# Performance work log

Hardware: AMD Instinct MI355X
Metric: run time of the kernel (lower is better)

Reference implementation:

```python
import jax, jax.numpy as jnp
import numpy as np

N = 100000   # nodes (single node type 'A')
C = 256      # hidden_channels
OUT = 128    # out_channels
E_RAND = 300000  # random edges; total E = N + E_RAND = 400000
LN_EPS = 1e-5


def _linear_params(key, in_c, out_c):
    kw, kb = jax.random.split(key)
    bound = 1.0 / np.sqrt(in_c)
    W = jax.random.uniform(kw, (out_c, in_c), minval=-bound, maxval=bound, dtype=jnp.float32)
    b = jax.random.uniform(kb, (out_c,), minval=-bound, maxval=bound, dtype=jnp.float32)
    return W, b


def _edges(key):
    # guarantee every node appears in both rows -> unique()/remap in the torch
    # code is the identity, so the subgraph equals the full graph
    k0, k1 = jax.random.split(key)
    base = jnp.arange(N, dtype=jnp.int64)
    row0 = jnp.concatenate([base, jax.random.randint(k0, (E_RAND,), 0, N, dtype=jnp.int64)])
    row1 = jnp.concatenate([base, jax.random.randint(k1, (E_RAND,), 0, N, dtype=jnp.int64)])
    return jnp.stack([row0, row1])


def setup_inputs() -> dict:
    key = jax.random.key(0)
    ks = jax.random.split(key, 12)
    x = jax.random.normal(ks[0], (N, C), dtype=jnp.float32)
    edge_index_r0 = _edges(ks[1])
    edge_index_r1 = _edges(ks[2])
    wl0, bl0 = _linear_params(ks[3], C, C)
    w00, b00 = _linear_params(ks[4], C, C)
    w10, b10 = _linear_params(ks[5], C, C)
    wl1, bl1 = _linear_params(ks[6], C, C)
    w01, b01 = _linear_params(ks[7], C, C)
    w11, b11 = _linear_params(ks[8], C, C)
    Wout, bout = _linear_params(ks[9], C, OUT)
    return dict(
        x=x, edge_index_r0=edge_index_r0, edge_index_r1=edge_index_r1,
        wl0=wl0, bl0=bl0, w00=w00, b00=b00, w10=w10, b10=b10,
        gate0=jnp.float32(0.5), lns0=jnp.ones((C,), jnp.float32), lnb0=jnp.zeros((C,), jnp.float32),
        wl1=wl1, bl1=bl1, w01=w01, b01=b01, w11=w11, b11=b11,
        gate1=jnp.float32(0.5), lns1=jnp.ones((C,), jnp.float32), lnb1=jnp.zeros((C,), jnp.float32),
        Wout=Wout, bout=bout,
    )


def _metapath_layer(x0, h, ei, wl, bl, w0, b0, w1, b1, gate, lns, lnb):
    n = h.shape[0]
    src, dst = ei[0], ei[1]
    # PyG flow='target_to_source', aggr='add': message x_j = h[edge_index[1]],
    # scatter-added at edge_index[0]
    agg = jax.ops.segment_sum(h[dst], src, num_segments=n)
    # original code normalizes by bincount of edge_index[1] (kept faithfully)
    deg = jax.ops.segment_sum(jnp.ones_like(dst, dtype=h.dtype), dst, num_segments=n)
    agg = agg / jnp.clip(deg, 1.0)[:, None]
    g = jax.nn.sigmoid(gate)
    out = (agg @ wl.T + bl) + (1.0 - g) * (h @ w0.T + b0) + g * (x0 @ w1.T + b1)
    out = jax.nn.relu(out)
    mu = out.mean(-1, keepdims=True)
    var = out.var(-1, keepdims=True)
    out = (out - mu) / jnp.sqrt(var + LN_EPS) * lns + lnb
    return out  # dropout is identity in eval mode


def reference(x, edge_index_r0, edge_index_r1,
              wl0, bl0, w00, b00, w10, b10, gate0, lns0, lnb0,
              wl1, bl1, w01, b01, w11, b11, gate1, lns1, lnb1,
              Wout, bout):
    x0 = jax.lax.stop_gradient(x)  # x0_dict is detached in the torch code
    h = x
    # metapath is processed in reverse: conv index 1 first, then conv index 0
    h = _metapath_layer(x0, h, edge_index_r1, wl1, bl1, w01, b01, w11, b11, gate1, lns1, lnb1)
    h = _metapath_layer(x0, h, edge_index_r0, wl0, bl0, w00, b00, w10, b10, gate0, lns0, lnb0)
    return h @ Wout.T + bout
```

## Files before the change

kernel.cpp:

```cpp
#include <hip/hip_runtime.h>

typedef unsigned short u16;
typedef unsigned int   u32;

typedef __attribute__((ext_vector_type(8))) __bf16 bf16x8;
typedef __attribute__((ext_vector_type(8))) unsigned short u16x8;
typedef __attribute__((ext_vector_type(4))) float  f32x4;

#define C      256
#define OUTC   128
#define LN_EPS 1e-5f

__device__ __forceinline__ float bf2f(u16 u) {
    u32 i = ((u32)u) << 16; float f; __builtin_memcpy(&f, &i, 4); return f;
}
__device__ __forceinline__ u16 f2bf(float f) {
    u32 i; __builtin_memcpy(&i, &f, 4);
    u32 r = (i + 0x7FFFu + ((i >> 16) & 1u)) >> 16;
    return (u16)r;
}
__device__ __forceinline__ void load_lds16(const void* g, void* l) {
    __builtin_amdgcn_global_load_lds((const __attribute__((address_space(1))) u32*)g,
                                     (__attribute__((address_space(3))) u32*)l, 16, 0, 0);
}
__device__ __forceinline__ int swz(int row) { return (row + (row >> 2)) & 3; }

__global__ void xcast_kernel(const float* __restrict__ x, u16* __restrict__ xb, size_t n8)
{
    size_t i = ((size_t)blockIdx.x * 256 + threadIdx.x);
    if (i >= n8) return;
    const float* p = x + i * 8;
    float4 v0 = *(const float4*)p;
    float4 v1 = *(const float4*)(p + 4);
    u16x8 o;
    o[0] = f2bf(v0.x); o[1] = f2bf(v0.y); o[2] = f2bf(v0.z); o[3] = f2bf(v0.w);
    o[4] = f2bf(v1.x); o[5] = f2bf(v1.y); o[6] = f2bf(v1.z); o[7] = f2bf(v1.w);
    *(u16x8*)(xb + i * 8) = o;
}

__global__ void prep_weights(const float* wl0, const float* w00, const float* w10,
                             const float* bl0, const float* b00, const float* b10,
                             const float* gate0,
                             const float* wl1, const float* w01, const float* w11,
                             const float* bl1, const float* b01, const float* b11,
                             const float* gate1,
                             const float* Wout,
                             u16* __restrict__ WcatA, u16* __restrict__ WcatB,
                             u16* __restrict__ Woutb, float* __restrict__ bcat)
{
    int idx = blockIdx.x * 256 + threadIdx.x;
    float gA = 1.f / (1.f + expf(-gate1[0]));
    float gB = 1.f / (1.f + expf(-gate0[0]));
    if (idx < 256 * 512) {
        int n = idx >> 9, k = idx & 511;
        float v;
        if (k < 256) v = wl1[n * 256 + k];
        else         v = (1.f - gA) * w01[n * 256 + (k - 256)] + gA * w11[n * 256 + (k - 256)];
        WcatA[idx] = f2bf(v);
    } else if (idx < 256 * 512 + 256 * 768) {
        int j = idx - 256 * 512;
        int n = j / 768, k = j - n * 768;
        float v;
        if (k < 256)      v = wl0[n * 256 + k];
        else if (k < 512) v = (1.f - gB) * w00[n * 256 + (k - 256)];
        else              v = gB * w10[n * 256 + (k - 512)];
        WcatB[j] = f2bf(v);
    } else {
        int j = idx - (256 * 512 + 256 * 768);
        if (j < OUTC * C) Woutb[j] = f2bf(Wout[j]);
    }
    if (idx < 512) {
        int nn = idx & 255;
        if (idx < 256) bcat[idx] = bl1[nn] + (1.f - gA) * b01[nn] + gA * b11[nn];
        else           bcat[idx] = bl0[nn] + (1.f - gB) * b00[nn] + gB * b10[nn];
    }
}

__global__ void count_edges(const int* __restrict__ ei, int* __restrict__ counts,
                            int* __restrict__ degcnt, int E, int Nn)
{
    int idx = blockIdx.x * 256 + threadIdx.x;
    if (idx >= E) return;
    int s = ei[idx], d = ei[E + idx];
    if ((unsigned)s >= (unsigned)Nn || (unsigned)d >= (unsigned)Nn) return;
    atomicAdd(counts + s, 1);
    atomicAdd(degcnt + d, 1);
}

__global__ void block_sums(const int* __restrict__ counts, int* __restrict__ partials, int n)
{
    int i = blockIdx.x * 256 + threadIdx.x;
    int v = (i < n) ? counts[i] : 0;
    #pragma unroll
    for (int off = 32; off; off >>= 1) v += __shfl_down(v, off, 64);
    __shared__ int ws[4];
    if ((threadIdx.x & 63) == 0) ws[threadIdx.x >> 6] = v;
    __syncthreads();
    if (threadIdx.x == 0) partials[blockIdx.x] = ws[0] + ws[1] + ws[2] + ws[3];
}

__global__ void scan_partials(int* __restrict__ partials, int nblk)
{
    __shared__ int buf[1024];
    int tid = threadIdx.x;
    int v = (tid < nblk) ? partials[tid] : 0;
    buf[tid] = v; __syncthreads();
    for (int off = 1; off < 1024; off <<= 1) {
        int t = (tid >= off) ? buf[tid - off] : 0;
        __syncthreads();
        buf[tid] += t;
        __syncthreads();
    }
    if (tid < nblk) partials[tid] = buf[tid] - v;
}

__global__ void make_offsets(int* __restrict__ counts_cursor, const int* __restrict__ partials,
                             int* __restrict__ offsets, int n)
{
    __shared__ int buf[256];
    int i = blockIdx.x * 256 + threadIdx.x;
    int cnt = (i < n) ? counts_cursor[i] : 0;
    buf[threadIdx.x] = cnt; __syncthreads();
    for (int off = 1; off < 256; off <<= 1) {
        int t = (threadIdx.x >= off) ? buf[threadIdx.x - off] : 0;
        __syncthreads();
        buf[threadIdx.x] += t;
        __syncthreads();
    }
    int off = partials[blockIdx.x] + buf[threadIdx.x] - cnt;
    if (i < n) {
        offsets[i] = off;
        counts_cursor[i] = off;
        if (i == n - 1) offsets[n] = off + cnt;
    }
}

__global__ void fill_edges(const int* __restrict__ ei, int* __restrict__ cursor,
                           int* __restrict__ edgedst, int E, int Nn)
{
    int idx = blockIdx.x * 256 + threadIdx.x;
    if (idx >= E) return;
    int s = ei[idx], d = ei[E + idx];
    if ((unsigned)s >= (unsigned)Nn || (unsigned)d >= (unsigned)Nn) return;
    int p = atomicAdd(cursor + s, 1);
    edgedst[p] = d;
}

__global__ __launch_bounds__(256) void gather_kernel(
    const int* __restrict__ offsets, const int* __restrict__ edgedst,
    const int* __restrict__ degcnt, const u16* __restrict__ h,
    u16* __restrict__ aggb, int Nn)
{
    int node = blockIdx.x * 4 + (threadIdx.x >> 6);
    if (node >= Nn) return;
    int lane = threadIdx.x & 63;
    int beg = offsets[node], end = offsets[node + 1];
    float4 acc = {0.f, 0.f, 0.f, 0.f};
    for (int e = beg; e < end; ++e) {
        int dst = edgedst[e];
        ushort4 v = *(const ushort4*)(h + (size_t)dst * C + lane * 4);
        acc.x += bf2f(v.x); acc.y += bf2f(v.y);
        acc.z += bf2f(v.z); acc.w += bf2f(v.w);
    }
    float inv = 1.0f / fmaxf((float)degcnt[node], 1.0f);
    ushort4 o;
    o.x = f2bf(acc.x * inv); o.y = f2bf(acc.y * inv);
    o.z = f2bf(acc.z * inv); o.w = f2bf(acc.w * inv);
    *(ushort4*)(aggb + (size_t)node * C + lane * 4) = o;
}

template <int NSEG>
__global__ __launch_bounds__(512, 4) void layer_gemm(
    const u16* __restrict__ s0, const u16* __restrict__ s1, const u16* __restrict__ s2,
    const u16* __restrict__ W,
    const float* __restrict__ bcat,
    const float* __restrict__ lns, const float* __restrict__ lnb,
    u16* __restrict__ Hout, int Nnodes)
{
    constexpr int WK = NSEG * 256;
    constexpr int KT = NSEG * 8;

    __shared__ u16 Alds[128 * 32];
    __shared__ u16 Blds[256 * 32];
    __shared__ float lnpart[128][4][2];

    const int tid  = threadIdx.x;
    const int wave = tid >> 6, lane = tid & 63;
    const int wave_m = wave & 1, wave_n = wave >> 1;
    const int q = lane >> 4, l15 = lane & 15;
    const int m0 = blockIdx.x * 128;

    const int srow = (wave << 4) + (lane >> 2);
    int anode = m0 + srow; if (anode >= Nnodes) anode = Nnodes - 1;
    const int asc = (lane & 3) ^ swz(srow);
    const size_t a_goff = (size_t)anode * C + asc * 8;
    u16* a_ldst = Alds + (wave << 9);

    const u16* bgp[2]; u16* bldst[2];
    #pragma unroll
    for (int i = 0; i < 2; ++i) {
        int cb = wave + i * 8;
        int brow = (cb << 4) + (lane >> 2);
        int bsc = (lane & 3) ^ swz(brow);
        bgp[i]   = W + brow * WK + bsc * 8;
        bldst[i] = Blds + (cb << 9);
    }

    int aoff[4], boff[4];
    #pragma unroll
    for (int t = 0; t < 4; ++t) {
        int ar = wave_m * 64 + t * 16 + l15;
        aoff[t] = ar * 32 + ((q ^ swz(ar)) << 3);
        int br = wave_n * 64 + t * 16 + l15;
        boff[t] = br * 32 + ((q ^ swz(br)) << 3);
    }

    f32x4 acc[4][4] = {};

    for (int kt = 0; kt < KT; ++kt) {
        const u16* Asrc = (kt < 8) ? s0 : ((NSEG == 2 || kt < 16) ? s1 : s2);
        load_lds16(Asrc + a_goff + ((kt & 7) << 5), a_ldst);
        int k0 = kt << 5;
        load_lds16(bgp[0] + k0, bldst[0]);
        load_lds16(bgp[1] + k0, bldst[1]);
        __syncthreads();

        bf16x8 af[4], bfr[4];
        #pragma unroll
        for (int t = 0; t < 4; ++t) af[t]  = *(const bf16x8*)&Alds[aoff[t]];
        #pragma unroll
        for (int f = 0; f < 4; ++f) bfr[f] = *(const bf16x8*)&Blds[boff[f]];
        #pragma unroll
        for (int t = 0; t < 4; ++t)
            #pragma unroll
            for (int f = 0; f < 4; ++f)
                acc[t][f] = __builtin_amdgcn_mfma_f32_16x16x32_bf16(af[t], bfr[f], acc[t][f], 0, 0, 0);
        __syncthreads();
    }

    float bias[4], lsc[4], lbi[4];
    #pragma unroll
    for (int f = 0; f < 4; ++f) {
        int n = wave_n * 64 + f * 16 + l15;
        bias[f] = bcat[n]; lsc[f] = lns[n]; lbi[f] = lnb[n];
    }
    #pragma unroll
    for (int t = 0; t < 4; ++t)
        #pragma unroll
        for (int r = 0; r < 4; ++r) {
            float p = 0.f, pp = 0.f;
            #pragma unroll
            for (int f = 0; f < 4; ++f) {
                float v = acc[t][f][r] + bias[f];
                v = fmaxf(v, 0.f);
                acc[t][f][r] = v;
                p += v; pp += v * v;
            }
            #pragma unroll
            for (int off = 1; off < 16; off <<= 1) {
                p  += __shfl_xor(p,  off, 16);
                pp += __shfl_xor(pp, off, 16);
            }
            if (l15 == 0) {
                int row = wave_m * 64 + t * 16 + q * 4 + r;
                lnpart[row][wave_n][0] = p;
                lnpart[row][wave_n][1] = pp;
            }
        }
    __syncthreads();
    #pragma unroll
    for (int t = 0; t < 4; ++t)
        #pragma unroll
        for (int r = 0; r < 4; ++r) {
            int row = wave_m * 64 + t * 16 + q * 4 + r;
            int node = m0 + row;
            if (node < Nnodes) {
                float S1 = lnpart[row][0][0] + lnpart[row][1][0]
                         + lnpart[row][2][0] + lnpart[row][3][0];
                float S2 = lnpart[row][0][1] + lnpart[row][1][1]
                         + lnpart[row][2][1] + lnpart[row][3][1];
                float mean = S1 * (1.f / 256.f);
                float var  = fmaxf(S2 * (1.f / 256.f) - mean * mean, 0.f);
                float rstd = rsqrtf(var + LN_EPS);
                u16* op = Hout + (size_t)node * C;
                #pragma unroll
                for (int f = 0; f < 4; ++f) {
                    int n = wave_n * 64 + f * 16 + l15;
                    op[n] = f2bf((acc[t][f][r] - mean) * rstd * lsc[f] + lbi[f]);
                }
            }
        }
}

__global__ __launch_bounds__(256) void final_gemm(
    const u16* __restrict__ A, const u16* __restrict__ W,
    const float* __restrict__ bout, float* __restrict__ out, int Nnodes)
{
    __shared__ u16 Alds[64 * 32];
    __shared__ u16 Blds[128 * 32];

    const int tid = threadIdx.x;
    const int wave = tid >> 6, lane = tid & 63;
    const int wave_m = wave & 1, wave_n = wave >> 1;
    const int q = lane >> 4, l15 = lane & 15;
    const int m0 = blockIdx.x * 64;

    int a_row  = wave * 16 + (lane >> 2);
    int a_node = m0 + a_row; if (a_node >= Nnodes) a_node = Nnodes - 1;
    const int kk8 = (lane & 3) * 8;
    const size_t a_off = (size_t)a_node * C + kk8;
    u16* AldsW = Alds + wave * 512;

    const u16* bg[2]; u16* bl[2];
    #pragma unroll
    for (int i = 0; i < 2; ++i) {
        int cb = wave * 2 + i;
        int n_row = cb * 16 + (lane >> 2);
        bg[i] = W + n_row * 256 + kk8;
        bl[i] = Blds + cb * 512;
    }

    f32x4 acc[2][4] = {};

    for (int kt = 0; kt < 8; ++kt) {
        int k0 = kt * 32;
        load_lds16(A + a_off + k0, AldsW);
        #pragma unroll
        for (int i = 0; i < 2; ++i) load_lds16(bg[i] + k0, bl[i]);
        __syncthreads();

        bf16x8 af[2], bfr[4];
        #pragma unroll
        for (int t = 0; t < 2; ++t)
            af[t] = *(const bf16x8*)&Alds[(wave_m * 32 + t * 16 + l15) * 32 + q * 8];
        #pragma unroll
        for (int f = 0; f < 4; ++f)
            bfr[f] = *(const bf16x8*)&Blds[(wave_n * 64 + f * 16 + l15) * 32 + q * 8];
        #pragma unroll
        for (int t = 0; t < 2; ++t)
            #pragma unroll
            for (int f = 0; f < 4; ++f)
                acc[t][f] = __builtin_amdgcn_mfma_f32_16x16x32_bf16(af[t], bfr[f], acc[t][f], 0, 0, 0);
        __syncthreads();
    }

    float bias[4];
    #pragma unroll
    for (int f = 0; f < 4; ++f) bias[f] = bout[wave_n * 64 + f * 16 + l15];
    #pragma unroll
    for (int t = 0; t < 2; ++t)
        #pragma unroll
        for (int r = 0; r < 4; ++r) {
            int row = wave_m * 32 + t * 16 + q * 4 + r;
            int node = m0 + row;
            if (node < Nnodes) {
                float* op = out + (size_t)node * OUTC;
                #pragma unroll
                for (int f = 0; f < 4; ++f) {
                    int n = wave_n * 64 + f * 16 + l15;
                    op[n] = acc[t][f][r] + bias[f];
                }
            }
        }
}

extern "C" void kernel_launch(void* const* d_in, const int* in_sizes, int n_in,
                              void* d_out, int out_size, void* d_ws, size_t ws_size,
                              hipStream_t stream)
{
    const float* x    = (const float*)d_in[0];
    const int*   ei0  = (const int*)d_in[1];
    const int*   ei1  = (const int*)d_in[2];
    const float* wl0  = (const float*)d_in[3];
    const float* bl0  = (const float*)d_in[4];
    const float* w00  = (const float*)d_in[5];
    const float* b00  = (const float*)d_in[6];
    const float* w10  = (const float*)d_in[7];
    const float* b10  = (const float*)d_in[8];
    const float* gate0= (const float*)d_in[9];
    const float* lns0 = (const float*)d_in[10];
    const float* lnb0 = (const float*)d_in[11];
    const float* wl1  = (const float*)d_in[12];
    const float* bl1  = (const float*)d_in[13];
    const float* w01  = (const float*)d_in[14];
    const float* b01  = (const float*)d_in[15];
    const float* w11  = (const float*)d_in[16];
    const float* b11  = (const float*)d_in[17];
    const float* gate1= (const float*)d_in[18];
    const float* lns1 = (const float*)d_in[19];
    const float* lnb1 = (const float*)d_in[20];
    const float* Wout = (const float*)d_in[21];
    const float* bout = (const float*)d_in[22];

    const int N = in_sizes[0] / C;
    const int E = in_sizes[1] / 2;

    char* w = (char*)d_ws;
    u16*   WcatA = (u16*)w;   w += (size_t)256 * 512 * 2;
    u16*   WcatB = (u16*)w;   w += (size_t)256 * 768 * 2;
    u16*   Woutb = (u16*)w;   w += (size_t)OUTC * C * 2;
    float* bcat  = (float*)w; w += 4096;
    int*   cnt1  = (int*)w;   w += (size_t)N * 4;
    int*   deg1  = (int*)w;   w += (size_t)N * 4;
    int*   cnt0  = (int*)w;   w += (size_t)N * 4;
    int*   deg0  = (int*)w;   w += (size_t)N * 4;
    int*   off1  = (int*)w;   w += (((size_t)(N + 1) * 4) + 255) & ~255ull;
    int*   off0  = (int*)w;   w += (((size_t)(N + 1) * 4) + 255) & ~255ull;
    int*   parts = (int*)w;   w += 4096;
    int*   ed1   = (int*)w;   w += (size_t)E * 4;
    int*   ed0   = (int*)w;   w += (size_t)E * 4;
    u16*   xb    = (u16*)w;   w += (size_t)N * C * 2;
    u16*   aggb  = (u16*)w;   w += (size_t)N * C * 2;
    u16*   h1    = (u16*)w;   w += (size_t)N * C * 2;

    const int eb_grid = (E + 255) / 256;
    const int nblk    = (N + 255) / 256;
    const int gt_grid = (N + 3) / 4;
    const int gm_grid = (N + 127) / 128;
    const int fg_grid = (N + 63) / 64;
    u16* h2 = (u16*)d_out;

    hipMemsetAsync(cnt1, 0, (size_t)4 * N * 4, stream);
    prep_weights<<<(256 * 512 + 256 * 768 + OUTC * C) / 256, 256, 0, stream>>>(
        wl0, w00, w10, bl0, b00, b10, gate0,
        wl1, w01, w11, bl1, b01, b11, gate1,
        Wout, WcatA, WcatB, Woutb, bcat);
    xcast_kernel<<<(int)(((size_t)N * C / 8 + 255) / 256), 256, 0, stream>>>(
        x, xb, (size_t)N * C / 8);

    count_edges<<<eb_grid, 256, 0, stream>>>(ei1, cnt1, deg1, E, N);
    count_edges<<<eb_grid, 256, 0, stream>>>(ei0, cnt0, deg0, E, N);
    block_sums<<<nblk, 256, 0, stream>>>(cnt1, parts, N);
    scan_partials<<<1, 1024, 0, stream>>>(parts, nblk);
    make_offsets<<<nblk, 256, 0, stream>>>(cnt1, parts, off1, N);
    fill_edges<<<eb_grid, 256, 0, stream>>>(ei1, cnt1, ed1, E, N);
    block_sums<<<nblk, 256, 0, stream>>>(cnt0, parts, N);
    scan_partials<<<1, 1024, 0, stream>>>(parts, nblk);
    make_offsets<<<nblk, 256, 0, stream>>>(cnt0, parts, off0, N);
    fill_edges<<<eb_grid, 256, 0, stream>>>(ei0, cnt0, ed0, E, N);

    gather_kernel<<<gt_grid, 256, 0, stream>>>(off1, ed1, deg1, xb, aggb, N);
    layer_gemm<2><<<gm_grid, 512, 0, stream>>>(aggb, xb, nullptr, WcatA, bcat,
                                               lns1, lnb1, h1, N);

    gather_kernel<<<gt_grid, 256, 0, stream>>>(off0, ed0, deg0, h1, aggb, N);
    layer_gemm<3><<<gm_grid, 512, 0, stream>>>(aggb, h1, xb, WcatB, bcat + C,
                                               lns0, lnb0, h2, N);

    final_gemm<<<fg_grid, 256, 0, stream>>>(h2, Woutb, bout, (float*)d_out, N);
}
```

Before: 592.3 us.

## Merge preprocessing launches, unroll gather loop, and retile final GEMM

Fuses the weight prep with the x bf16 cast, and batches the CSR-building kernels for both edge sets into single launches using block-index dispatch, with separate partial buffers. The gather loop is unrolled by two with independent accumulators to expose more memory-level parallelism. The final output GEMM moves to 128-row tiles with 512 threads and a swizzled LDS layout. Fewer launches and more overlap are the aim, at the cost of more register pressure in the reworked kernels.

Result: faster. 556.7 us (-6.0%).

```diff
diff --git a/kernel.cpp b/kernel.cpp
--- a/kernel.cpp
+++ b/kernel.cpp
@@ -25,29 +25,30 @@
 }
 __device__ __forceinline__ int swz(int row) { return (row + (row >> 2)) & 3; }
 
-__global__ void xcast_kernel(const float* __restrict__ x, u16* __restrict__ xb, size_t n8)
-{
-    size_t i = ((size_t)blockIdx.x * 256 + threadIdx.x);
-    if (i >= n8) return;
-    const float* p = x + i * 8;
-    float4 v0 = *(const float4*)p;
-    float4 v1 = *(const float4*)(p + 4);
-    u16x8 o;
-    o[0] = f2bf(v0.x); o[1] = f2bf(v0.y); o[2] = f2bf(v0.z); o[3] = f2bf(v0.w);
-    o[4] = f2bf(v1.x); o[5] = f2bf(v1.y); o[6] = f2bf(v1.z); o[7] = f2bf(v1.w);
-    *(u16x8*)(xb + i * 8) = o;
-}
-
-__global__ void prep_weights(const float* wl0, const float* w00, const float* w10,
-                             const float* bl0, const float* b00, const float* b10,
-                             const float* gate0,
-                             const float* wl1, const float* w01, const float* w11,
-                             const float* bl1, const float* b01, const float* b11,
-                             const float* gate1,
-                             const float* Wout,
-                             u16* __restrict__ WcatA, u16* __restrict__ WcatB,
-                             u16* __restrict__ Woutb, float* __restrict__ bcat)
-{
+#define PREP_BLK 1408
+__global__ void prep_combo(const float* wl0, const float* w00, const float* w10,
+                           const float* bl0, const float* b00, const float* b10,
+                           const float* gate0,
+                           const float* wl1, const float* w01, const float* w11,
+                           const float* bl1, const float* b01, const float* b11,
+                           const float* gate1,
+                           const float* Wout, const float* x,
+                           u16* __restrict__ WcatA, u16* __restrict__ WcatB,
+                           u16* __restrict__ Woutb, float* __restrict__ bcat,
+                           u16* __restrict__ xb, size_t n8)
+{
+    if (blockIdx.x >= PREP_BLK) {
+        size_t i = ((size_t)(blockIdx.x - PREP_BLK) * 256 + threadIdx.x);
+        if (i >= n8) return;
+        const float* p = x + i * 8;
+        float4 v0 = *(const float4*)p;
+        float4 v1 = *(const float4*)(p + 4);
+        u16x8 o;
+        o[0] = f2bf(v0.x); o[1] = f2bf(v0.y); o[2] = f2bf(v0.z); o[3] = f2bf(v0.w);
+        o[4] = f2bf(v1.x); o[5] = f2bf(v1.y); o[6] = f2bf(v1.z); o[7] = f2bf(v1.w);
+        *(u16x8*)(xb + i * 8) = o;
+        return;
+    }
     int idx = blockIdx.x * 256 + threadIdx.x;
     float gA = 1.f / (1.f + expf(-gate1[0]));
     float gB = 1.f / (1.f + expf(-gate0[0]));
@@ -76,31 +77,44 @@
     }
 }
 
-__global__ void count_edges(const int* __restrict__ ei, int* __restrict__ counts,
-                            int* __restrict__ degcnt, int E, int Nn)
-{
-    int idx = blockIdx.x * 256 + threadIdx.x;
+__global__ void count_edges2(const int* __restrict__ ei1, const int* __restrict__ ei0,
+                             int* __restrict__ cnt1, int* __restrict__ deg1,
+                             int* __restrict__ cnt0, int* __restrict__ deg0,
+                             int E, int Nn, int ebg)
+{
+    int b = blockIdx.x;
+    const int* ei; int *cnt, *deg;
+    if (b < ebg) { ei = ei1; cnt = cnt1; deg = deg1; }
+    else         { b -= ebg; ei = ei0; cnt = cnt0; deg = deg0; }
+    int idx = b * 256 + threadIdx.x;
     if (idx >= E) return;
     int s = ei[idx], d = ei[E + idx];
     if ((unsigned)s >= (unsigned)Nn || (unsigned)d >= (unsigned)Nn) return;
-    atomicAdd(counts + s, 1);
-    atomicAdd(degcnt + d, 1);
-}
-
-__global__ void block_sums(const int* __restrict__ counts, int* __restrict__ partials, int n)
-{
-    int i = blockIdx.x * 256 + threadIdx.x;
+    atomicAdd(cnt + s, 1);
+    atomicAdd(deg + d, 1);
+}
+
+__global__ void block_sums2(const int* __restrict__ cnt1, const int* __restrict__ cnt0,
+                            int* __restrict__ parts1, int* __restrict__ parts0,
+                            int n, int nblk)
+{
+    int b = blockIdx.x;
+    const int* counts; int* partials;
+    if (b < nblk) { counts = cnt1; partials = parts1; }
+    else          { b -= nblk; counts = cnt0; partials = parts0; }
+    int i = b * 256 + threadIdx.x;
     int v = (i < n) ? counts[i] : 0;
     #pragma unroll
     for (int off = 32; off; off >>= 1) v += __shfl_down(v, off, 64);
     __shared__ int ws[4];
     if ((threadIdx.x & 63) == 0) ws[threadIdx.x >> 6] = v;
     __syncthreads();
-    if (threadIdx.x == 0) partials[blockIdx.x] = ws[0] + ws[1] + ws[2] + ws[3];
-}
-
-__global__ void scan_partials(int* __restrict__ partials, int nblk)
-{
+    if (threadIdx.x == 0) partials[b] = ws[0] + ws[1] + ws[2] + ws[3];
+}
+
+__global__ void scan_partials2(int* __restrict__ parts1, int* __restrict__ parts0, int nblk)
+{
+    int* partials = blockIdx.x ? parts0 : parts1;
     __shared__ int buf[1024];
     int tid = threadIdx.x;
     int v = (tid < nblk) ? partials[tid] : 0;
@@ -114,11 +128,17 @@
     if (tid < nblk) partials[tid] = buf[tid] - v;
 }
 
-__global__ void make_offsets(int* __restrict__ counts_cursor, const int* __restrict__ partials,
-                             int* __restrict__ offsets, int n)
-{
+__global__ void make_offsets2(int* __restrict__ cnt1, int* __restrict__ cnt0,
+                              const int* __restrict__ parts1, const int* __restrict__ parts0,
+                              int* __restrict__ off1a, int* __restrict__ off0a,
+                              int n, int nblk)
+{
+    int b = blockIdx.x;
+    int* counts_cursor; const int* partials; int* offsets;
+    if (b < nblk) { counts_cursor = cnt1; partials = parts1; offsets = off1a; }
+    else          { b -= nblk; counts_cursor = cnt0; partials = parts0; offsets = off0a; }
     __shared__ int buf[256];
-    int i = blockIdx.x * 256 + threadIdx.x;
+    int i = b * 256 + threadIdx.x;
     int cnt = (i < n) ? counts_cursor[i] : 0;
     buf[threadIdx.x] = cnt; __syncthreads();
     for (int off = 1; off < 256; off <<= 1) {
@@ -127,7 +147,7 @@
         buf[threadIdx.x] += t;
         __syncthreads();
     }
-    int off = partials[blockIdx.x] + buf[threadIdx.x] - cnt;
+    int off = partials[b] + buf[threadIdx.x] - cnt;
     if (i < n) {
         offsets[i] = off;
         counts_cursor[i] = off;
@@ -135,10 +155,16 @@
     }
 }
 
-__global__ void fill_edges(const int* __restrict__ ei, int* __restrict__ cursor,
-                           int* __restrict__ edgedst, int E, int Nn)
-{
-    int idx = blockIdx.x * 256 + threadIdx.x;
+__global__ void fill_edges2(const int* __restrict__ ei1, const int* __restrict__ ei0,
+                            int* __restrict__ cur1, int* __restrict__ cur0,
+                            int* __restrict__ ed1, int* __restrict__ ed0,
+                            int E, int Nn, int ebg)
+{
+    int b = blockIdx.x;
+    const int* ei; int *cursor, *edgedst;
+    if (b < ebg) { ei = ei1; cursor = cur1; edgedst = ed1; }
+    else         { b -= ebg; ei = ei0; cursor = cur0; edgedst = ed0; }
+    int idx = b * 256 + threadIdx.x;
     if (idx >= E) return;
     int s = ei[idx], d = ei[E + idx];
     if ((unsigned)s >= (unsigned)Nn || (unsigned)d >= (unsigned)Nn) return;
@@ -155,17 +181,24 @@
     if (node >= Nn) return;
     int lane = threadIdx.x & 63;
     int beg = offsets[node], end = offsets[node + 1];
-    float4 acc = {0.f, 0.f, 0.f, 0.f};
-    for (int e = beg; e < end; ++e) {
-        int dst = edgedst[e];
-        ushort4 v = *(const ushort4*)(h + (size_t)dst * C + lane * 4);
-        acc.x += bf2f(v.x); acc.y += bf2f(v.y);
-        acc.z += bf2f(v.z); acc.w += bf2f(v.w);
+    float4 a0 = {0.f, 0.f, 0.f, 0.f}, a1 = {0.f, 0.f, 0.f, 0.f};
+    int e = beg;
+    for (; e + 1 < end; e += 2) {
+        int d0 = edgedst[e], d1 = edgedst[e + 1];
+        ushort4 v0 = *(const ushort4*)(h + (size_t)d0 * C + lane * 4);
+        ushort4 v1 = *(const ushort4*)(h + (size_t)d1 * C + lane * 4);
+        a0.x += bf2f(v0.x); a0.y += bf2f(v0.y); a0.z += bf2f(v0.z); a0.w += bf2f(v0.w);
+        a1.x += bf2f(v1.x); a1.y += bf2f(v1.y); a1.z += bf2f(v1.z); a1.w += bf2f(v1.w);
+    }
+    if (e < end) {
+        int d0 = edgedst[e];
+        ushort4 v0 = *(const ushort4*)(h + (size_t)d0 * C + lane * 4);
+        a0.x += bf2f(v0.x); a0.y += bf2f(v0.y); a0.z += bf2f(v0.z); a0.w += bf2f(v0.w);
     }
     float inv = 1.0f / fmaxf((float)degcnt[node], 1.0f);
     ushort4 o;
-    o.x = f2bf(acc.x * inv); o.y = f2bf(acc.y * inv);
-    o.z = f2bf(acc.z * inv); o.w = f2bf(acc.w * inv);
+    o.x = f2bf((a0.x + a1.x) * inv); o.y = f2bf((a0.y + a1.y) * inv);
+    o.z = f2bf((a0.z + a1.z) * inv); o.w = f2bf((a0.w + a1.w) * inv);
     *(ushort4*)(aggb + (size_t)node * C + lane * 4) = o;
 }
 
@@ -292,72 +325,76 @@
         }
 }
 
-__global__ __launch_bounds__(256) void final_gemm(
+__global__ __launch_bounds__(512, 4) void final_gemm(
     const u16* __restrict__ A, const u16* __restrict__ W,
     const float* __restrict__ bout, float* __restrict__ out, int Nnodes)
 {
-    __shared__ u16 Alds[64 * 32];
+    __shared__ u16 Alds[128 * 32];
     __shared__ u16 Blds[128 * 32];
 
     const int tid = threadIdx.x;
     const int wave = tid >> 6, lane = tid & 63;
     const int wave_m = wave & 1, wave_n = wave >> 1;
     const int q = lane >> 4, l15 = lane & 15;
-    const int m0 = blockIdx.x * 64;
-
-    int a_row  = wave * 16 + (lane >> 2);
-    int a_node = m0 + a_row; if (a_node >= Nnodes) a_node = Nnodes - 1;
-    const int kk8 = (lane & 3) * 8;
-    const size_t a_off = (size_t)a_node * C + kk8;
-    u16* AldsW = Alds + wave * 512;
-
-    const u16* bg[2]; u16* bl[2];
-    #pragma unroll
-    for (int i = 0; i < 2; ++i) {
-        int cb = wave * 2 + i;
-        int n_row = cb * 16 + (lane >> 2);
-        bg[i] = W + n_row * 256 + kk8;
-        bl[i] = Blds + cb * 512;
-    }
-
-    f32x4 acc[2][4] = {};
+    const int m0 = blockIdx.x * 128;
+
+    const int srow = (wave << 4) + (lane >> 2);
+    int anode = m0 + srow; if (anode >= Nnodes) anode = Nnodes - 1;
+    const int asc = (lane & 3) ^ swz(srow);
+    const size_t a_goff = (size_t)anode * C + asc * 8;
+    u16* a_ldst = Alds + (wave << 9);
+
+    const int bsc = (lane & 3) ^ swz(srow);
+    const u16* bgp = W + srow * C + bsc * 8;
+    u16* bldst = Blds + (wave << 9);
+
+    int aoff[4], boff[2];
+    #pragma unroll
+    for (int t = 0; t < 4; ++t) {
+        int ar = wave_m * 64 + t * 16 + l15;
+        aoff[t] = ar * 32 + ((q ^ swz(ar)) << 3);
+    }
+    #pragma unroll
+    for (int f = 0; f < 2; ++f) {
+        int br = wave_n * 32 + f * 16 + l15;
+        boff[f] = br * 32 + ((q ^ swz(br)) << 3);
+    }
+
+    f32x4 acc[4][2] = {};
 
     for (int kt = 0; kt < 8; ++kt) {
-        int k0 = kt * 32;
-        load_lds16(A + a_off + k0, AldsW);
-        #pragma unroll
-        for (int i = 0; i < 2; ++i) load_lds16(bg[i] + k0, bl[i]);
-        __syncthreads();
-
-        bf16x8 af[2], bfr[4];
-        #pragma unroll
-        for (int t = 0; t < 2; ++t)
-            af[t] = *(const bf16x8*)&Alds[(wave_m * 32 + t * 16 + l15) * 32 + q * 8];
-        #pragma unroll
-        for (int f = 0; f < 4; ++f)
-            bfr[f] = *(const bf16x8*)&Blds[(wave_n * 64 + f * 16 + l15) * 32 + q * 8];
-        #pragma unroll
-        for (int t = 0; t < 2; ++t)
+        int k0 = kt << 5;
+        load_lds16(A + a_goff + k0, a_ldst);
+        load_lds16(bgp + k0, bldst);
+        __syncthreads();
+
+        bf16x8 af[4], bfr[2];
+        #pragma unroll
+        for (int t = 0; t < 4; ++t) af[t]  = *(const bf16x8*)&Alds[aoff[t]];
+        #pragma unroll
+        for (int f = 0; f < 2; ++f) bfr[f] = *(const bf16x8*)&Blds[boff[f]];
+        #pragma unroll
+        for (int t = 0; t < 4; ++t)
             #pragma unroll
-            for (int f = 0; f < 4; ++f)
+            for (int f = 0; f < 2; ++f)
                 acc[t][f] = __builtin_amdgcn_mfma_f32_16x16x32_bf16(af[t], bfr[f], acc[t][f], 0, 0, 0);
         __syncthreads();
     }
 
-    float bias[4];
-    #pragma unroll
-    for (int f = 0; f < 4; ++f) bias[f] = bout[wave_n * 64 + f * 16 + l15];
-    #pragma unroll
-    for (int t = 0; t < 2; ++t)
+    float bias[2];
+    #pragma unroll
+    for (int f = 0; f < 2; ++f) bias[f] = bout[wave_n * 32 + f * 16 + l15];
+    #pragma unroll
+    for (int t = 0; t < 4; ++t)
         #pragma unroll
         for (int r = 0; r < 4; ++r) {
-            int row = wave_m * 32 + t * 16 + q * 4 + r;
+            int row = wave_m * 64 + t * 16 + q * 4 + r;
             int node = m0 + row;
             if (node < Nnodes) {
                 float* op = out + (size_t)node * OUTC;
                 #pragma unroll
-                for (int f = 0; f < 4; ++f) {
-                    int n = wave_n * 64 + f * 16 + l15;
+                for (int f = 0; f < 2; ++f) {
+                    int n = wave_n * 32 + f * 16 + l15;
                     op[n] = acc[t][f][r] + bias[f];
                 }
             }
@@ -406,7 +443,8 @@
     int*   deg0  = (int*)w;   w += (size_t)N * 4;
     int*   off1  = (int*)w;   w += (((size_t)(N + 1) * 4) + 255) & ~255ull;
     int*   off0  = (int*)w;   w += (((size_t)(N + 1) * 4) + 255) & ~255ull;
-    int*   parts = (int*)w;   w += 4096;
+    int*   parts1= (int*)w;   w += 4096;
+    int*   parts0= (int*)w;   w += 4096;
     int*   ed1   = (int*)w;   w += (size_t)E * 4;
     int*   ed0   = (int*)w;   w += (size_t)E * 4;
     u16*   xb    = (u16*)w;   w += (size_t)N * C * 2;
@@ -417,27 +455,21 @@
     const int nblk    = (N + 255) / 256;
     const int gt_grid = (N + 3) / 4;
     const int gm_grid = (N + 127) / 128;
-    const int fg_grid = (N + 63) / 64;
+    const size_t n8   = (size_t)N * C / 8;
+    const int xc_blk  = (int)((n8 + 255) / 256);
     u16* h2 = (u16*)d_out;
 
     hipMemsetAsync(cnt1, 0, (size_t)4 * N * 4, stream);
-    prep_weights<<<(256 * 512 + 256 * 768 + OUTC * C) / 256, 256, 0, stream>>>(
+    prep_combo<<<PREP_BLK + xc_blk, 256, 0, stream>>>(
         wl0, w00, w10, bl0, b00, b10, gate0,
         wl1, w01, w11, bl1, b01, b11, gate1,
-        Wout, WcatA, WcatB, Woutb, bcat);
-    xcast_kernel<<<(int)(((size_t)N * C / 8 + 255) / 256), 256, 0, stream>>>(
-        x, xb, (size_t)N * C / 8);
-
-    count_edges<<<eb_grid, 256, 0, stream>>>(ei1, cnt1, deg1, E, N);
-    count_edges<<<eb_grid, 256, 0, stream>>>(ei0, cnt0, deg0, E, N);
-    block_sums<<<nblk, 256, 0, stream>>>(cnt1, parts, N);
-    scan_partials<<<1, 1024, 0, stream>>>(parts, nblk);
-    make_offsets<<<nblk, 256, 0, stream>>>(cnt1, parts, off1, N);
-    fill_edges<<<eb_grid, 256, 0, stream>>>(ei1, cnt1, ed1, E, N);
-    block_sums<<<nblk, 256, 0, stream>>>(cnt0, parts, N);
-    scan_partials<<<1, 1024, 0, stream>>>(parts, nblk);
-    make_offsets<<<nblk, 256, 0, stream>>>(cnt0, parts, off0, N);
-    fill_edges<<<eb_grid, 256, 0, stream>>>(ei0, cnt0, ed0, E, N);
+        Wout, x, WcatA, WcatB, Woutb, bcat, xb, n8);
+
+    count_edges2 <<<2 * eb_grid, 256, 0, stream>>>(ei1, ei0, cnt1, deg1, cnt0, deg0, E, N, eb_grid);
+    block_sums2  <<<2 * nblk, 256, 0, stream>>>(cnt1, cnt0, parts1, parts0, N, nblk);
+    scan_partials2<<<2, 1024, 0, stream>>>(parts1, parts0, nblk);
+    make_offsets2<<<2 * nblk, 256, 0, stream>>>(cnt1, cnt0, parts1, parts0, off1, off0, N, nblk);
+    fill_edges2  <<<2 * eb_grid, 256, 0, stream>>>(ei1, ei0, cnt1, cnt0, ed1, ed0, E, N, eb_grid);
 
     gather_kernel<<<gt_grid, 256, 0, stream>>>(off1, ed1, deg1, xb, aggb, N);
     layer_gemm<2><<<gm_grid, 512, 0, stream>>>(aggb, xb, nullptr, WcatA, bcat,
@@ -447,5 +479,5 @@
     layer_gemm<3><<<gm_grid, 512, 0, stream>>>(aggb, h1, xb, WcatB, bcat + C,
                                                lns0, lnb0, h2, N);
 
-    final_gemm<<<fg_grid, 256, 0, stream>>>(h2, Woutb, bout, (float*)d_out, N);
-}
+    final_gemm<<<gm_grid, 512, 0, stream>>>(h2, Woutb, bout, (float*)d_out, N);
+}
```
